# Kernel tuning notes

Measured on AMD Instinct MI355X. Metric: run time of the kernel, lower is better.

The kernel has to match this reference:

```python
import jax, jax.numpy as jnp
import numpy as np

N = 4096
NFEAT = 512
NHID = 60
NCLASS = 4


def setup_inputs() -> dict:
    key = jax.random.key(0)
    ks = jax.random.split(key, 12)
    x = jax.random.normal(ks[0], (N, NFEAT), dtype=jnp.float32)
    # sparse-ish binary adjacency (sub_adj), symmetric not required by the module
    sub_adj = (jax.random.uniform(ks[1], (N, N)) < 0.002).astype(jnp.float32)
    # P_vec: init to ones (torch.sub in reset_parameters is non-inplace, so it stays ones)
    P_vec = jnp.ones((N * (N + 1) // 2,), dtype=jnp.float32)
    s1 = 1.0 / np.sqrt(NFEAT)
    s2 = 1.0 / np.sqrt(NHID)
    W1 = jax.random.normal(ks[2], (NFEAT, NHID), dtype=jnp.float32) * s1
    b1 = jax.random.normal(ks[3], (NHID,), dtype=jnp.float32) * 0.01
    W2 = jax.random.normal(ks[4], (NHID, NHID), dtype=jnp.float32) * s2
    b2 = jax.random.normal(ks[5], (NHID,), dtype=jnp.float32) * 0.01
    W3 = jax.random.normal(ks[6], (NHID, NHID), dtype=jnp.float32) * s2
    b3 = jax.random.normal(ks[7], (NHID,), dtype=jnp.float32) * 0.01
    lin_w = jax.random.normal(ks[8], (NHID, NCLASS), dtype=jnp.float32) * s2
    lin_b = jax.random.normal(ks[9], (NCLASS,), dtype=jnp.float32) * 0.01
    return {"x": x, "sub_adj": sub_adj, "P_vec": P_vec,
            "W1": W1, "b1": b1, "W2": W2, "b2": b2, "W3": W3, "b3": b3,
            "lin_w": lin_w, "lin_b": lin_b}


def reference(x, sub_adj, P_vec, W1, b1, W2, b2, W3, b3, lin_w, lin_b):
    n = sub_adj.shape[0]
    # scatter P_vec into lower triangle (incl. diagonal), then symmetrize
    il, jl = jnp.tril_indices(n)
    M = jnp.zeros((n, n), dtype=P_vec.dtype).at[il, jl].set(P_vec)
    P_hat_symm = M + M.T - jnp.diag(jnp.diag(M))
    # perturbed adjacency with self-loops
    A_tilde = jax.nn.sigmoid(P_hat_symm) * sub_adj + jnp.eye(n, dtype=P_vec.dtype)
    # degree (column sums, matching python sum(adj)); detached in the original
    d = jax.lax.stop_gradient(jnp.sum(A_tilde, axis=0))
    d_inv_sqrt = jnp.where(d > 0, d ** -0.5, 0.0)  # isinf -> 0
    # D^{-1/2} A D^{-1/2} without materializing diag matrices
    norm_adj = d_inv_sqrt[:, None] * A_tilde * d_inv_sqrt[None, :]
    # 3 GCN layers: spmm(norm_adj, x @ W) + b
    h1 = jax.nn.relu(norm_adj @ (x @ W1) + b1)
    h2 = jax.nn.relu(norm_adj @ (h1 @ W2) + b2)
    h3 = norm_adj @ (h2 @ W3) + b3
    logits = h3 @ lin_w + lin_b  # dropout is identity in eval / p=0
    return jax.nn.log_softmax(logits, axis=1)
```

## Files before the change

### kernel.cpp

```cpp
#include <hip/hip_runtime.h>
#include <math.h>

#define NN 4096
#define NFEAT 512
#define NHID 60
#define NCLASS 4
#define CAP 96
#define GSTRIDE 64
#define QCAP 128
#define XWBLK (NN / 4)
#define SCANBLK (NN * NN / 4 / 2048)

__device__ __forceinline__ void scan_f4(const float4 av4, int f4idx,
                                        const float* __restrict__ P,
                                        float* __restrict__ dcol,
                                        int* __restrict__ cnt,
                                        int* __restrict__ cols,
                                        float* __restrict__ vals) {
    const float av[4] = {av4.x, av4.y, av4.z, av4.w};
    const int e0 = f4idx * 4;
    #pragma unroll
    for (int q = 0; q < 4; ++q) {
        if (av[q] != 0.f) {
            const int e = e0 + q;
            const int i = e >> 12;
            const int j = e & (NN - 1);
            const int hi = i > j ? i : j;
            const int lo = i > j ? j : i;
            const float pv = P[((hi * (hi + 1)) >> 1) + lo];
            const float s = av[q] / (1.f + __expf(-pv));
            atomicAdd(&dcol[j], s);
            const int pos = atomicAdd(&cnt[i], 1);
            if (pos < CAP) { cols[i * CAP + pos] = j; vals[i * CAP + pos] = s; }
        }
    }
}

__global__ __launch_bounds__(256) void k_scan_xw(const float* __restrict__ x,
                                                 const float* __restrict__ adj,
                                                 const float* __restrict__ P,
                                                 const float* __restrict__ W1,
                                                 float* __restrict__ dcol,
                                                 int* __restrict__ cnt,
                                                 int* __restrict__ cols,
                                                 float* __restrict__ vals,
                                                 float* __restrict__ g1) {
    __shared__ float part[1024];
    __shared__ int wq[4][QCAP];
    __shared__ int wq_n[4];
    const int tid = threadIdx.x;
    const int w = tid >> 6, lane = tid & 63;

    if (blockIdx.x >= XWBLK) {
        if (tid < 4) wq_n[tid] = 0;
        __syncthreads();
        const int base = (blockIdx.x - XWBLK) * 2048 + tid;
        const uint4* adj4 = (const uint4*)adj;
        uint4 a[8];
        #pragma unroll
        for (int u = 0; u < 8; ++u) a[u] = adj4[base + u * 256];
        #pragma unroll
        for (int u = 0; u < 8; ++u) {
            if (a[u].x | a[u].y | a[u].z | a[u].w) {
                const int p = atomicAdd(&wq_n[w], 1);
                if (p < QCAP) wq[w][p] = base + u * 256;
                else {
                    const uint4 v = a[u];
                    const float4 f = make_float4(__uint_as_float(v.x), __uint_as_float(v.y),
                                                 __uint_as_float(v.z), __uint_as_float(v.w));
                    scan_f4(f, base + u * 256, P, dcol, cnt, cols, vals);
                }
            }
        }
        __syncthreads();
        const int n = min(wq_n[w], QCAP);
        for (int l = lane; l < n; l += 64) {
            const int idx = wq[w][l];
            scan_f4(((const float4*)adj)[idx], idx, P, dcol, cnt, cols, vals);
        }
        return;
    }

    const int c = lane < NHID ? lane : 0;
    const int row0 = blockIdx.x * 4;
    const int k0 = w * (NFEAT / 4);
    const float* x0 = x + (row0 + 0) * NFEAT;
    const float* x1 = x + (row0 + 1) * NFEAT;
    const float* x2 = x + (row0 + 2) * NFEAT;
    const float* x3 = x + (row0 + 3) * NFEAT;
    float a0 = 0.f, a1 = 0.f, a2 = 0.f, a3 = 0.f;
    for (int k = k0; k < k0 + NFEAT / 4; k += 4) {
        const float4 xv0 = *(const float4*)(x0 + k);
        const float4 xv1 = *(const float4*)(x1 + k);
        const float4 xv2 = *(const float4*)(x2 + k);
        const float4 xv3 = *(const float4*)(x3 + k);
        const float w0 = W1[(k + 0) * NHID + c];
        const float w1 = W1[(k + 1) * NHID + c];
        const float w2 = W1[(k + 2) * NHID + c];
        const float w3 = W1[(k + 3) * NHID + c];
        a0 = fmaf(xv0.x, w0, fmaf(xv0.y, w1, fmaf(xv0.z, w2, fmaf(xv0.w, w3, a0))));
        a1 = fmaf(xv1.x, w0, fmaf(xv1.y, w1, fmaf(xv1.z, w2, fmaf(xv1.w, w3, a1))));
        a2 = fmaf(xv2.x, w0, fmaf(xv2.y, w1, fmaf(xv2.z, w2, fmaf(xv2.w, w3, a2))));
        a3 = fmaf(xv3.x, w0, fmaf(xv3.y, w1, fmaf(xv3.z, w2, fmaf(xv3.w, w3, a3))));
    }
    part[(w * 4 + 0) * 64 + lane] = a0;
    part[(w * 4 + 1) * 64 + lane] = a1;
    part[(w * 4 + 2) * 64 + lane] = a2;
    part[(w * 4 + 3) * 64 + lane] = a3;
    __syncthreads();
    const float o = part[(0 * 4 + w) * 64 + lane] + part[(1 * 4 + w) * 64 + lane]
                  + part[(2 * 4 + w) * 64 + lane] + part[(3 * 4 + w) * 64 + lane];
    g1[(row0 + w) * GSTRIDE + lane] = (lane < NHID) ? o : 0.f;
}

__device__ __forceinline__ float spmm_row(const float* __restrict__ gin,
                                          const float* __restrict__ dcol,
                                          const int* __restrict__ cnt,
                                          const int* __restrict__ cols,
                                          const float* __restrict__ vals,
                                          int i, int lane, float di) {
    const int nn = min(cnt[i], CAP);
    float acc = gin[i * GSTRIDE + lane] * di;
    const int4*   c4 = (const int4*)(cols + i * CAP);
    const float4* v4 = (const float4*)(vals + i * CAP);
    int e = 0;
    for (; e + 4 <= nn; e += 4) {
        const int4   jj = c4[e >> 2];
        const float4 vv = v4[e >> 2];
        const float f0 = vv.x * rsqrtf(1.f + dcol[jj.x]);
        const float f1 = vv.y * rsqrtf(1.f + dcol[jj.y]);
        const float f2 = vv.z * rsqrtf(1.f + dcol[jj.z]);
        const float f3 = vv.w * rsqrtf(1.f + dcol[jj.w]);
        const float g0 = gin[jj.x * GSTRIDE + lane];
        const float g1 = gin[jj.y * GSTRIDE + lane];
        const float g2 = gin[jj.z * GSTRIDE + lane];
        const float g3 = gin[jj.w * GSTRIDE + lane];
        acc = fmaf(f0, g0, fmaf(f1, g1, fmaf(f2, g2, fmaf(f3, g3, acc))));
    }
    for (; e < nn; ++e) {
        const int j = cols[i * CAP + e];
        const float f = vals[i * CAP + e] * rsqrtf(1.f + dcol[j]);
        acc = fmaf(f, gin[j * GSTRIDE + lane], acc);
    }
    return acc * di;
}

__global__ __launch_bounds__(256) void k_layer(const float* __restrict__ gin,
                                               float* __restrict__ gout,
                                               const float* __restrict__ dcol,
                                               const int* __restrict__ cnt,
                                               const int* __restrict__ cols,
                                               const float* __restrict__ vals,
                                               const float* __restrict__ bias,
                                               const float* __restrict__ W) {
    __shared__ float Ws[NHID * NHID];
    __shared__ float hs[256];
    const int tid = threadIdx.x;
    for (int t = tid; t < NHID * NHID; t += 256) Ws[t] = W[t];
    const int w = tid >> 6, lane = tid & 63;
    const int i = blockIdx.x * 4 + w;
    const float di = rsqrtf(1.f + dcol[i]);
    const float acc = spmm_row(gin, dcol, cnt, cols, vals, i, lane, di);
    hs[w * 64 + lane] = (lane < NHID) ? fmaxf(acc + bias[lane], 0.f) : 0.f;
    __syncthreads();
    const int c = lane < NHID ? lane : 0;
    float o = 0.f;
    #pragma unroll 6
    for (int k = 0; k < NHID; ++k)
        o = fmaf(hs[w * 64 + k], Ws[k * NHID + c], o);
    gout[i * GSTRIDE + lane] = (lane < NHID) ? o : 0.f;
}

__global__ __launch_bounds__(256) void k_final(const float* __restrict__ gin,
                                               float* __restrict__ out,
                                               const float* __restrict__ dcol,
                                               const int* __restrict__ cnt,
                                               const int* __restrict__ cols,
                                               const float* __restrict__ vals,
                                               const float* __restrict__ b3,
                                               const float* __restrict__ lw,
                                               const float* __restrict__ lb) {
    __shared__ float lws[NHID * NCLASS];
    __shared__ float hs[256];
    const int tid = threadIdx.x;
    for (int t = tid; t < NHID * NCLASS; t += 256) lws[t] = lw[t];
    const int w = tid >> 6, lane = tid & 63;
    const int i = blockIdx.x * 4 + w;
    const float di = rsqrtf(1.f + dcol[i]);
    const float acc = spmm_row(gin, dcol, cnt, cols, vals, i, lane, di);
    hs[w * 64 + lane] = (lane < NHID) ? acc + b3[lane] : 0.f;
    __syncthreads();
    if (lane < NCLASS) {
        float o = lb[lane];
        #pragma unroll 4
        for (int k = 0; k < NHID; ++k)
            o = fmaf(hs[w * 64 + k], lws[k * NCLASS + lane], o);
        float m = fmaxf(o, __shfl_xor(o, 1));
        m = fmaxf(m, __shfl_xor(m, 2));
        const float ex = __expf(o - m);
        float ss = ex + __shfl_xor(ex, 1);
        ss += __shfl_xor(ss, 2);
        out[i * NCLASS + lane] = o - m - __logf(ss);
    }
}

extern "C" void kernel_launch(void* const* d_in, const int* in_sizes, int n_in,
                              void* d_out, int out_size, void* d_ws, size_t ws_size,
                              hipStream_t stream) {
    const float* x   = (const float*)d_in[0];
    const float* adj = (const float*)d_in[1];
    const float* P   = (const float*)d_in[2];
    const float* W1  = (const float*)d_in[3];
    const float* b1  = (const float*)d_in[4];
    const float* W2  = (const float*)d_in[5];
    const float* b2  = (const float*)d_in[6];
    const float* W3  = (const float*)d_in[7];
    const float* b3  = (const float*)d_in[8];
    const float* lw  = (const float*)d_in[9];
    const float* lb  = (const float*)d_in[10];
    float* out = (float*)d_out;

    char* ws = (char*)d_ws;
    float* dcol = (float*)(ws);
    int*   cnt  = (int*)(ws + 16384);
    int*   cols = (int*)(ws + 32768);
    float* vals = (float*)(ws + 32768 + 1572864);
    float* bufA = (float*)(ws + 32768 + 2 * 1572864);
    float* bufB = (float*)(ws + 32768 + 2 * 1572864 + 1048576);

    hipMemsetAsync(ws, 0, 32768, stream);

    k_scan_xw<<<XWBLK + SCANBLK, 256, 0, stream>>>(x, adj, P, W1,
                                                   dcol, cnt, cols, vals, bufA);
    k_layer<<<NN / 4, 256, 0, stream>>>(bufA, bufB, dcol, cnt, cols, vals, b1, W2);
    k_layer<<<NN / 4, 256, 0, stream>>>(bufB, bufA, dcol, cnt, cols, vals, b2, W3);
    k_final<<<NN / 4, 256, 0, stream>>>(bufA, out, dcol, cnt, cols, vals, b3, lw, lb);
}
```

Baseline: 189.8 us.

## Compact nonzero adjacency edges to a global list and process them in a separate kernel

The adjacency scan blocks now only stream the dense matrix and push the flat indices of individual nonzero elements into a per-block shared queue. The queue is then appended to a global edge list with one atomic per block. A new k_edges kernel gathers P, computes the sigmoid and does the degree and CSR-insert atomics for each listed edge. This keeps the scattered P loads and global atomics out of the bandwidth-bound streaming pass, at the cost of an extra launch and global traffic for the edge list. The edge weight is now the bare sigmoid without multiplying by the adjacency value, which assumes the adjacency is binary.

```diff
diff --git a/kernel.cpp b/kernel.cpp
--- a/kernel.cpp
+++ b/kernel.cpp
@@ -7,52 +7,46 @@
 #define NCLASS 4
 #define CAP 96
 #define GSTRIDE 64
-#define QCAP 128
+#define QCAP 256
+#define GECAP 65536
 #define XWBLK (NN / 4)
 #define SCANBLK (NN * NN / 4 / 2048)
 
-__device__ __forceinline__ void scan_f4(const float4 av4, int f4idx,
-                                        const float* __restrict__ P,
-                                        float* __restrict__ dcol,
-                                        int* __restrict__ cnt,
-                                        int* __restrict__ cols,
-                                        float* __restrict__ vals) {
-    const float av[4] = {av4.x, av4.y, av4.z, av4.w};
-    const int e0 = f4idx * 4;
-    #pragma unroll
-    for (int q = 0; q < 4; ++q) {
-        if (av[q] != 0.f) {
-            const int e = e0 + q;
-            const int i = e >> 12;
-            const int j = e & (NN - 1);
-            const int hi = i > j ? i : j;
-            const int lo = i > j ? j : i;
-            const float pv = P[((hi * (hi + 1)) >> 1) + lo];
-            const float s = av[q] / (1.f + __expf(-pv));
-            atomicAdd(&dcol[j], s);
-            const int pos = atomicAdd(&cnt[i], 1);
-            if (pos < CAP) { cols[i * CAP + pos] = j; vals[i * CAP + pos] = s; }
-        }
-    }
-}
-
-__global__ __launch_bounds__(256) void k_scan_xw(const float* __restrict__ x,
-                                                 const float* __restrict__ adj,
-                                                 const float* __restrict__ P,
-                                                 const float* __restrict__ W1,
-                                                 float* __restrict__ dcol,
-                                                 int* __restrict__ cnt,
-                                                 int* __restrict__ cols,
-                                                 float* __restrict__ vals,
-                                                 float* __restrict__ g1) {
+__device__ __forceinline__ void scan_elem(int e,
+                                          const float* __restrict__ P,
+                                          float* __restrict__ dcol,
+                                          int* __restrict__ cnt,
+                                          int* __restrict__ cols,
+                                          float* __restrict__ vals) {
+    const int i = e >> 12;
+    const int j = e & (NN - 1);
+    const int hi = i > j ? i : j;
+    const int lo = i > j ? j : i;
+    const float pv = P[((hi * (hi + 1)) >> 1) + lo];
+    const float s = 1.f / (1.f + __expf(-pv));
+    atomicAdd(&dcol[j], s);
+    const int pos = atomicAdd(&cnt[i], 1);
+    if (pos < CAP) { cols[i * CAP + pos] = j; vals[i * CAP + pos] = s; }
+}
+
+__global__ __launch_bounds__(256) void k_stream_xw(const float* __restrict__ x,
+                                                   const float* __restrict__ adj,
+                                                   const float* __restrict__ P,
+                                                   const float* __restrict__ W1,
+                                                   float* __restrict__ dcol,
+                                                   int* __restrict__ cnt,
+                                                   int* __restrict__ cols,
+                                                   float* __restrict__ vals,
+                                                   int* __restrict__ nedge,
+                                                   int* __restrict__ gedges,
+                                                   float* __restrict__ g1) {
     __shared__ float part[1024];
-    __shared__ int wq[4][QCAP];
-    __shared__ int wq_n[4];
+    __shared__ int q[QCAP];
+    __shared__ int qn, qbase;
     const int tid = threadIdx.x;
-    const int w = tid >> 6, lane = tid & 63;
 
     if (blockIdx.x >= XWBLK) {
-        if (tid < 4) wq_n[tid] = 0;
+        if (tid == 0) qn = 0;
         __syncthreads();
         const int base = (blockIdx.x - XWBLK) * 2048 + tid;
         const uint4* adj4 = (const uint4*)adj;
@@ -61,26 +55,33 @@
         for (int u = 0; u < 8; ++u) a[u] = adj4[base + u * 256];
         #pragma unroll
         for (int u = 0; u < 8; ++u) {
-            if (a[u].x | a[u].y | a[u].z | a[u].w) {
-                const int p = atomicAdd(&wq_n[w], 1);
-                if (p < QCAP) wq[w][p] = base + u * 256;
-                else {
-                    const uint4 v = a[u];
-                    const float4 f = make_float4(__uint_as_float(v.x), __uint_as_float(v.y),
-                                                 __uint_as_float(v.z), __uint_as_float(v.w));
-                    scan_f4(f, base + u * 256, P, dcol, cnt, cols, vals);
+            const uint4 v = a[u];
+            if (v.x | v.y | v.z | v.w) {
+                const int e0 = (base + u * 256) * 4;
+                const unsigned m[4] = {v.x, v.y, v.z, v.w};
+                #pragma unroll
+                for (int qq = 0; qq < 4; ++qq) {
+                    if (m[qq]) {
+                        const int p = atomicAdd(&qn, 1);
+                        if (p < QCAP) q[p] = e0 + qq;
+                        else scan_elem(e0 + qq, P, dcol, cnt, cols, vals);
+                    }
                 }
             }
         }
         __syncthreads();
-        const int n = min(wq_n[w], QCAP);
-        for (int l = lane; l < n; l += 64) {
-            const int idx = wq[w][l];
-            scan_f4(((const float4*)adj)[idx], idx, P, dcol, cnt, cols, vals);
+        const int n = min(qn, QCAP);
+        if (tid == 0) qbase = atomicAdd(nedge, n);
+        __syncthreads();
+        for (int t = tid; t < n; t += 256) {
+            const int dst = qbase + t;
+            if (dst < GECAP) gedges[dst] = q[t];
+            else scan_elem(q[t], P, dcol, cnt, cols, vals);
         }
         return;
     }
 
+    const int w = tid >> 6, lane = tid & 63;
     const int c = lane < NHID ? lane : 0;
     const int row0 = blockIdx.x * 4;
     const int k0 = w * (NFEAT / 4);
@@ -111,6 +112,18 @@
     const float o = part[(0 * 4 + w) * 64 + lane] + part[(1 * 4 + w) * 64 + lane]
                   + part[(2 * 4 + w) * 64 + lane] + part[(3 * 4 + w) * 64 + lane];
     g1[(row0 + w) * GSTRIDE + lane] = (lane < NHID) ? o : 0.f;
+}
+
+__global__ __launch_bounds__(256) void k_edges(const float* __restrict__ P,
+                                               float* __restrict__ dcol,
+                                               int* __restrict__ cnt,
+                                               int* __restrict__ cols,
+                                               float* __restrict__ vals,
+                                               const int* __restrict__ nedge,
+                                               const int* __restrict__ gedges) {
+    const int t = blockIdx.x * 256 + threadIdx.x;
+    const int n = min(*nedge, GECAP);
+    if (t < n) scan_elem(gedges[t], P, dcol, cnt, cols, vals);
 }
 
 __device__ __forceinline__ float spmm_row(const float* __restrict__ gin,
@@ -221,17 +234,20 @@
     float* out = (float*)d_out;
 
     char* ws = (char*)d_ws;
-    float* dcol = (float*)(ws);
-    int*   cnt  = (int*)(ws + 16384);
-    int*   cols = (int*)(ws + 32768);
-    float* vals = (float*)(ws + 32768 + 1572864);
-    float* bufA = (float*)(ws + 32768 + 2 * 1572864);
-    float* bufB = (float*)(ws + 32768 + 2 * 1572864 + 1048576);
-
-    hipMemsetAsync(ws, 0, 32768, stream);
-
-    k_scan_xw<<<XWBLK + SCANBLK, 256, 0, stream>>>(x, adj, P, W1,
-                                                   dcol, cnt, cols, vals, bufA);
+    float* dcol   = (float*)(ws);
+    int*   cnt    = (int*)(ws + 16384);
+    int*   nedge  = (int*)(ws + 32768);
+    int*   gedges = (int*)(ws + 33024);
+    int*   cols   = (int*)(ws + 295168);
+    float* vals   = (float*)(ws + 295168 + 1572864);
+    float* bufA   = (float*)(ws + 295168 + 2 * 1572864);
+    float* bufB   = (float*)(ws + 295168 + 2 * 1572864 + 1048576);
+
+    hipMemsetAsync(ws, 0, 33024, stream);
+
+    k_stream_xw<<<XWBLK + SCANBLK, 256, 0, stream>>>(x, adj, P, W1, dcol, cnt,
+                                                     cols, vals, nedge, gedges, bufA);
+    k_edges<<<GECAP / 256, 256, 0, stream>>>(P, dcol, cnt, cols, vals, nedge, gedges);
     k_layer<<<NN / 4, 256, 0, stream>>>(bufA, bufB, dcol, cnt, cols, vals, b1, W2);
     k_layer<<<NN / 4, 256, 0, stream>>>(bufB, bufA, dcol, cnt, cols, vals, b2, W3);
     k_final<<<NN / 4, 256, 0, stream>>>(bufA, out, dcol, cnt, cols, vals, b3, lw, lb);
```

Result: slower. 199.2 us (+5.0%).
